# Kernel tuning notes

Measured on AMD Instinct MI355X. Metric: run time of the kernel, lower is better.

## Reference

```python
import jax, jax.numpy as jnp
import numpy as np
from jax import lax

B, T, N_INPUT = 64, 2048, 257
HIDDEN = 32
N_OUTPUT = 10


def setup_inputs() -> dict:
    key = jax.random.key(0)
    ks = jax.random.split(key, 7)
    return {
        "specs": jax.random.normal(ks[0], (B, T, N_INPUT), dtype=jnp.float32),
        "W_ih": jax.random.normal(ks[1], (4 * HIDDEN, N_INPUT), dtype=jnp.float32) * 0.05,
        "W_hh": jax.random.normal(ks[2], (4 * HIDDEN, HIDDEN), dtype=jnp.float32) * 0.05,
        "b_ih": jax.random.normal(ks[3], (4 * HIDDEN,), dtype=jnp.float32) * 0.05,
        "b_hh": jax.random.normal(ks[4], (4 * HIDDEN,), dtype=jnp.float32) * 0.05,
        "W_out": jax.random.normal(ks[5], (N_OUTPUT, HIDDEN), dtype=jnp.float32) * 0.05,
        "b_out": jax.random.normal(ks[6], (N_OUTPUT,), dtype=jnp.float32) * 0.05,
    }


def reference(specs, W_ih, W_hh, b_ih, b_hh, W_out, b_out):
    # specs: [B, T, n_input]. PyTorch LSTMCell, gate order (i, f, g, o).
    b, t, _ = specs.shape
    h0 = jnp.zeros((b, HIDDEN), dtype=specs.dtype)
    c0 = jnp.zeros((b, HIDDEN), dtype=specs.dtype)
    # Precompute input projection for all timesteps in one GEMM: [B, T, 4H]
    x_proj = jnp.einsum("bti,gi->btg", specs, W_ih) + b_ih + b_hh
    x_proj = jnp.swapaxes(x_proj, 0, 1)  # [T, B, 4H] for scan

    def step(carry, xg):
        h, c = carry
        gates = xg + h @ W_hh.T  # [B, 4H]
        i, f, g, o = jnp.split(gates, 4, axis=-1)
        i = jax.nn.sigmoid(i)
        f = jax.nn.sigmoid(f)
        g = jnp.tanh(g)
        o = jax.nn.sigmoid(o)
        c = f * c + i * g
        h = o * jnp.tanh(c)
        return (h, c), None

    (hn, _), _ = lax.scan(step, (h0, c0), x_proj)
    logits = jax.nn.relu(hn) @ W_out.T + b_out  # [B, n_output]
    return jax.nn.log_softmax(logits, axis=1)
```

## Files before the change

### kernel.cpp

```cpp
#include <hip/hip_runtime.h>

#define B_SZ 64
#define T_LEN 2048
#define NIN 257
#define HID 32
#define G4 128
#define NOUT 10

#define TBT 128
#define PAD 34
#define CH 8
#define NSCAN 64
#define NGEMMP 128
#define NTILE 1024
#define TPB 16

#define SC_SIG  -1.44269504f
#define SC_TANH -2.88539008f

typedef int v2i __attribute__((ext_vector_type(2)));
typedef unsigned long long u64;

__device__ __forceinline__ void pkfma2(float2& acc, float2 w, u64 h2) {
  asm("v_pk_fma_f32 %0, %1, %2, %0" : "+v"(acc) : "v"(w), "s"(h2));
}

__device__ __forceinline__ float2 pkadd(float2 a, float2 b) {
  float2 d;
  asm("v_pk_add_f32 %0, %1, %2" : "=v"(d) : "v"(a), "v"(b));
  return d;
}

__device__ __forceinline__ void gemm_tile(
    const float* __restrict__ A, const float* __restrict__ W,
    const float* __restrict__ b_ih, const float* __restrict__ b_hh,
    float* __restrict__ C, int bt0, float* sA, float* sB)
{
  const int tid = threadIdx.x;
  const int gt = tid & 15;
  const int btt = tid >> 4;
  float acc[8][8];
#pragma unroll
  for (int i = 0; i < 8; ++i)
#pragma unroll
    for (int j = 0; j < 8; ++j) acc[i][j] = 0.f;

  for (int kc = 0; kc < 8; ++kc) {
    const int k0 = kc * 32;
    __syncthreads();
#pragma unroll
    for (int i = 0; i < 16; ++i) {
      int s = i * 256 + tid;
      int r = s >> 5, cc = s & 31;
      sA[r * PAD + cc] = A[(size_t)(bt0 + r) * NIN + k0 + cc];
      sB[r * PAD + cc] = W[(size_t)r * NIN + k0 + cc];
    }
    __syncthreads();
#pragma unroll
    for (int k2 = 0; k2 < 16; ++k2) {
      float2 a2[8], b2[8];
#pragma unroll
      for (int i = 0; i < 8; ++i)
        a2[i] = *(const float2*)&sA[(btt + 16 * i) * PAD + 2 * k2];
#pragma unroll
      for (int j = 0; j < 8; ++j)
        b2[j] = *(const float2*)&sB[(gt + 16 * j) * PAD + 2 * k2];
#pragma unroll
      for (int i = 0; i < 8; ++i)
#pragma unroll
        for (int j = 0; j < 8; ++j) {
          acc[i][j] = fmaf(a2[i].x, b2[j].x, acc[i][j]);
          acc[i][j] = fmaf(a2[i].y, b2[j].y, acc[i][j]);
        }
    }
  }
  {
    float a[8], bb[8];
#pragma unroll
    for (int i = 0; i < 8; ++i) a[i] = A[(size_t)(bt0 + btt + 16 * i) * NIN + 256];
#pragma unroll
    for (int j = 0; j < 8; ++j) bb[j] = W[(size_t)(gt + 16 * j) * NIN + 256];
#pragma unroll
    for (int i = 0; i < 8; ++i)
#pragma unroll
      for (int j = 0; j < 8; ++j) acc[i][j] += a[i] * bb[j];
  }
  float bias[8], sc[8];
  int off[8];
#pragma unroll
  for (int j = 0; j < 8; ++j) {
    const int col = gt + 16 * j;
    bias[j] = b_ih[col] + b_hh[col];
    sc[j] = ((col >> 5) == 2) ? SC_TANH : SC_SIG;
    off[j] = ((col & 63) << 1) + (col >> 6);
  }
#pragma unroll
  for (int i = 0; i < 8; ++i) {
    size_t row = (size_t)(bt0 + btt + 16 * i) * G4;
#pragma unroll
    for (int j = 0; j < 8; ++j) C[row + off[j]] = (acc[i][j] + bias[j]) * sc[j];
  }
}

__global__ __launch_bounds__(256) void fused(
    const float* __restrict__ A,
    const float* __restrict__ W,
    const float* __restrict__ b_ih,
    const float* __restrict__ b_hh,
    const float* __restrict__ W_hh,
    const float* __restrict__ W_out,
    const float* __restrict__ b_out,
    float* __restrict__ out,
    float* __restrict__ xproj,
    int* __restrict__ flags,
    int nowait)
{
  __shared__ float sA[TBT * PAD];
  __shared__ float sB[G4 * PAD];
  const int bid = blockIdx.x;

  if (bid >= NSCAN) {
    const int p = bid - NSCAN;
    for (int idx = p; idx < NTILE; idx += NGEMMP) {
      const int ti = idx >> 6, bb = idx & 63;
      const int bt0 = bb * T_LEN + ti * TBT;
      gemm_tile(A, W, b_ih, b_hh, xproj, bt0, sA, sB);
      __threadfence();
      __syncthreads();
      if (threadIdx.x == 0)
        __hip_atomic_store(&flags[idx], 1, __ATOMIC_RELEASE, __HIP_MEMORY_SCOPE_AGENT);
    }
    return;
  }

  if (threadIdx.x >= 64) return;
  __builtin_amdgcn_s_setprio(3);
  const int b = bid;
  const int l = threadIdx.x;

  const float wsB = (l < HID) ? SC_TANH : SC_SIG;
  float2 wA[16], wB[16];
#pragma unroll
  for (int j = 0; j < 16; j += 2) {
    float4 v0 = *(const float4*)&W_hh[l * HID + 2 * j];
    wA[j]     = make_float2(v0.x * SC_SIG, v0.y * SC_SIG);
    wA[j + 1] = make_float2(v0.z * SC_SIG, v0.w * SC_SIG);
    float4 v1 = *(const float4*)&W_hh[(l + 64) * HID + 2 * j];
    wB[j]     = make_float2(v1.x * wsB, v1.y * wsB);
    wB[j + 1] = make_float2(v1.z * wsB, v1.w * wsB);
  }

  float c = 0.f, h = 0.f;
  u64 hp[16];
#pragma unroll
  for (int k = 0; k < 16; ++k) hp[k] = 0ull;

  const float2* xb2 = (const float2*)(xproj + (size_t)b * T_LEN * G4);

  auto step = [&](float xa, float xg) {
    float2 aA[4], aB[4];
    aA[0] = make_float2(xa, 0.f);
    aB[0] = make_float2(xg, 0.f);
#pragma unroll
    for (int q = 1; q < 4; ++q) {
      aA[q] = make_float2(0.f, 0.f);
      aB[q] = make_float2(0.f, 0.f);
    }
#pragma unroll
    for (int j = 0; j < 16; j += 4) {
#pragma unroll
      for (int q = 0; q < 4; ++q) {
        pkfma2(aA[q], wA[j + q], hp[j + q]);
        pkfma2(aB[q], wB[j + q], hp[j + q]);
      }
    }
    float2 tA = pkadd(pkadd(aA[0], aA[1]), pkadd(aA[2], aA[3]));
    float2 tB = pkadd(pkadd(aB[0], aB[1]), pkadd(aB[2], aB[3]));
    float accA = tA.x + tA.y;
    float accB = tB.x + tB.y;
    float actA = __builtin_amdgcn_rcpf(1.f + __builtin_amdgcn_exp2f(accA));
    float sB2  = __builtin_amdgcn_rcpf(1.f + __builtin_amdgcn_exp2f(accB));
    float actA2 = actA + actA;
    float prod  = fmaf(actA2, sB2, -actA);
    v2i sw = __builtin_amdgcn_permlane32_swap(0, __float_as_int(prod), false, false);
    float pr = __int_as_float(sw[0]);
    c = fmaf(actA, c, pr);
    float t  = __builtin_amdgcn_rcpf(1.f + __builtin_amdgcn_exp2f(SC_TANH * c));
    float s2 = sB2 + sB2;
    h = fmaf(s2, t, -sB2);
#pragma unroll
    for (int k = 0; k < 16; ++k) {
      unsigned lo = (unsigned)__builtin_amdgcn_readlane(__float_as_int(h), 32 + 2 * k);
      unsigned hi = (unsigned)__builtin_amdgcn_readlane(__float_as_int(h), 33 + 2 * k);
      hp[k] = (u64)lo | ((u64)hi << 32);
    }
  };

  float2 X0[CH], X1[CH];
#define LOADC2(X, P) do { _Pragma("unroll") \
  for (int i = 0; i < CH; ++i) X[i] = (P)[i * 64]; } while (0)
#define STEPS(X) do { _Pragma("unroll") \
  for (int i = 0; i < CH; ++i) step(X[i].x, X[i].y); } while (0)

  for (int ti = 0; ti < TPB; ++ti) {
    if (!nowait) {
      while (__hip_atomic_load(&flags[ti * 64 + b], __ATOMIC_ACQUIRE,
                               __HIP_MEMORY_SCOPE_AGENT) == 0)
        __builtin_amdgcn_s_sleep(2);
    }
    const float2* xt = xb2 + (size_t)ti * TBT * 64 + l;
    LOADC2(X0, xt);
#pragma unroll 1
    for (int ch = 0; ch < TBT / CH; ch += 2) {
      const float2* s1 = xt + (size_t)(ch + 1) * CH * 64;
      LOADC2(X1, s1);
      STEPS(X0);
      if (ch + 2 < TBT / CH) {
        const float2* s2 = xt + (size_t)(ch + 2) * CH * 64;
        LOADC2(X0, s2);
      }
      STEPS(X1);
    }
  }

  float hf[HID];
#pragma unroll
  for (int k = 0; k < HID; ++k)
    hf[k] = __int_as_float(__builtin_amdgcn_readlane(__float_as_int(h), 32 + k));
  float logit = 0.f;
  if (l < NOUT) {
    logit = b_out[l];
#pragma unroll
    for (int j = 0; j < HID; ++j) logit += fmaxf(hf[j], 0.f) * W_out[l * HID + j];
  }
  float m = -1e30f;
#pragma unroll
  for (int n = 0; n < NOUT; ++n) m = fmaxf(m, __shfl(logit, n));
  float s = 0.f;
#pragma unroll
  for (int n = 0; n < NOUT; ++n)
    s += __builtin_amdgcn_exp2f(1.44269504089f * (__shfl(logit, n) - m));
  if (l < NOUT)
    out[b * NOUT + l] = logit - m - 0.69314718056f * __builtin_amdgcn_logf(s);
}

__global__ __launch_bounds__(256) void xproj_gemm(
    const float* __restrict__ A, const float* __restrict__ W,
    const float* __restrict__ b_ih, const float* __restrict__ b_hh,
    float* __restrict__ C)
{
  __shared__ float sA[TBT * PAD];
  __shared__ float sB[G4 * PAD];
  const int idx = blockIdx.x;
  const int ti = idx >> 6, bb = idx & 63;
  gemm_tile(A, W, b_ih, b_hh, C, bb * T_LEN + ti * TBT, sA, sB);
}

extern "C" void kernel_launch(void* const* d_in, const int* in_sizes, int n_in,
                              void* d_out, int out_size, void* d_ws, size_t ws_size,
                              hipStream_t stream) {
  const float* specs = (const float*)d_in[0];
  const float* W_ih  = (const float*)d_in[1];
  const float* W_hh  = (const float*)d_in[2];
  const float* b_ih  = (const float*)d_in[3];
  const float* b_hh  = (const float*)d_in[4];
  const float* W_out = (const float*)d_in[5];
  const float* b_out = (const float*)d_in[6];
  float* outp  = (float*)d_out;
  float* xproj = (float*)d_ws;
  const size_t xbytes = (size_t)B_SZ * T_LEN * G4 * 4;

  if (ws_size >= xbytes + NTILE * sizeof(int)) {
    int* flags = (int*)((char*)d_ws + xbytes);
    (void)hipMemsetAsync(flags, 0, NTILE * sizeof(int), stream);
    fused<<<NSCAN + NGEMMP, 256, 0, stream>>>(specs, W_ih, b_ih, b_hh, W_hh,
                                              W_out, b_out, outp, xproj, flags, 0);
  } else {
    xproj_gemm<<<NTILE, 256, 0, stream>>>(specs, W_ih, b_ih, b_hh, xproj);
    fused<<<NSCAN, 256, 0, stream>>>(specs, W_ih, b_ih, b_hh, W_hh,
                                     W_out, b_out, outp, xproj, (int*)xproj , 1);
  }
}
```

Baseline: 565.9 us.

## Use fp16 dot2 for recurrent matvec and halve h broadcast readlanes

Converts the pre-scaled recurrent weights and the broadcast hidden state to packed fp16 and replaces the packed fp32 FMAs with v_dot2_f32_f16, so each instruction handles two products with fp32 accumulation. A DPP move pairs neighbouring h values before packing, which cuts the per-step readlane count from 32 to 16. The cell state is kept pre-scaled so the tanh argument needs no multiply. This shortens the serial per-timestep chain but lowers the precision of h and W_hh to fp16, which may cause accuracy drift over 2048 steps.

```diff
diff --git a/kernel.cpp b/kernel.cpp
--- a/kernel.cpp
+++ b/kernel.cpp
@@ -21,15 +21,11 @@
 typedef int v2i __attribute__((ext_vector_type(2)));
 typedef unsigned long long u64;
 
-__device__ __forceinline__ void pkfma2(float2& acc, float2 w, u64 h2) {
-  asm("v_pk_fma_f32 %0, %1, %2, %0" : "+v"(acc) : "v"(w), "s"(h2));
-}
-
-__device__ __forceinline__ float2 pkadd(float2 a, float2 b) {
-  float2 d;
-  asm("v_pk_add_f32 %0, %1, %2" : "=v"(d) : "v"(a), "v"(b));
-  return d;
-}
+#define DOT2(acc, w, hpk) \
+  asm("v_dot2_f32_f16 %0, %1, %2, %0" : "+v"(acc) : "v"(w), "s"(hpk))
+
+#define PKF16(dst, a, b) \
+  asm("v_cvt_pkrtz_f16_f32 %0, %1, %2" : "=v"(dst) : "v"(a), "v"(b))
 
 __device__ __forceinline__ void gemm_tile(
     const float* __restrict__ A, const float* __restrict__ W,
@@ -139,61 +135,57 @@
   const int l = threadIdx.x;
 
   const float wsB = (l < HID) ? SC_TANH : SC_SIG;
-  float2 wA[16], wB[16];
+  unsigned wA[16], wB[16];
 #pragma unroll
   for (int j = 0; j < 16; j += 2) {
     float4 v0 = *(const float4*)&W_hh[l * HID + 2 * j];
-    wA[j]     = make_float2(v0.x * SC_SIG, v0.y * SC_SIG);
-    wA[j + 1] = make_float2(v0.z * SC_SIG, v0.w * SC_SIG);
+    PKF16(wA[j],     v0.x * SC_SIG, v0.y * SC_SIG);
+    PKF16(wA[j + 1], v0.z * SC_SIG, v0.w * SC_SIG);
     float4 v1 = *(const float4*)&W_hh[(l + 64) * HID + 2 * j];
-    wB[j]     = make_float2(v1.x * wsB, v1.y * wsB);
-    wB[j + 1] = make_float2(v1.z * wsB, v1.w * wsB);
+    PKF16(wB[j],     v1.x * wsB, v1.y * wsB);
+    PKF16(wB[j + 1], v1.z * wsB, v1.w * wsB);
   }
 
   float c = 0.f, h = 0.f;
-  u64 hp[16];
-#pragma unroll
-  for (int k = 0; k < 16; ++k) hp[k] = 0ull;
+  unsigned hp[16];
+#pragma unroll
+  for (int k = 0; k < 16; ++k) hp[k] = 0u;
 
   const float2* xb2 = (const float2*)(xproj + (size_t)b * T_LEN * G4);
 
   auto step = [&](float xa, float xg) {
-    float2 aA[4], aB[4];
-    aA[0] = make_float2(xa, 0.f);
-    aB[0] = make_float2(xg, 0.f);
-#pragma unroll
-    for (int q = 1; q < 4; ++q) {
-      aA[q] = make_float2(0.f, 0.f);
-      aB[q] = make_float2(0.f, 0.f);
-    }
-#pragma unroll
-    for (int j = 0; j < 16; j += 4) {
-#pragma unroll
-      for (int q = 0; q < 4; ++q) {
-        pkfma2(aA[q], wA[j + q], hp[j + q]);
-        pkfma2(aB[q], wB[j + q], hp[j + q]);
-      }
-    }
-    float2 tA = pkadd(pkadd(aA[0], aA[1]), pkadd(aA[2], aA[3]));
-    float2 tB = pkadd(pkadd(aB[0], aB[1]), pkadd(aB[2], aB[3]));
-    float accA = tA.x + tA.y;
-    float accB = tB.x + tB.y;
+    float aA0 = xa,  aA1 = 0.f, aA2 = 0.f, aA3 = 0.f;
+    float aB0 = xg,  aB1 = 0.f, aB2 = 0.f, aB3 = 0.f;
+#pragma unroll
+    for (int j = 0; j < 4; ++j) {
+      DOT2(aA0, wA[j],      hp[j]);
+      DOT2(aA1, wA[4 + j],  hp[4 + j]);
+      DOT2(aA2, wA[8 + j],  hp[8 + j]);
+      DOT2(aA3, wA[12 + j], hp[12 + j]);
+      DOT2(aB0, wB[j],      hp[j]);
+      DOT2(aB1, wB[4 + j],  hp[4 + j]);
+      DOT2(aB2, wB[8 + j],  hp[8 + j]);
+      DOT2(aB3, wB[12 + j], hp[12 + j]);
+    }
+    float accA = (aA0 + aA1) + (aA2 + aA3);
+    float accB = (aB0 + aB1) + (aB2 + aB3);
     float actA = __builtin_amdgcn_rcpf(1.f + __builtin_amdgcn_exp2f(accA));
     float sB2  = __builtin_amdgcn_rcpf(1.f + __builtin_amdgcn_exp2f(accB));
-    float actA2 = actA + actA;
-    float prod  = fmaf(actA2, sB2, -actA);
+    float m1 = actA * (2.f * SC_TANH);
+    float sh = sB2 - 0.5f;
+    float prod = m1 * sh;
     v2i sw = __builtin_amdgcn_permlane32_swap(0, __float_as_int(prod), false, false);
     float pr = __int_as_float(sw[0]);
     c = fmaf(actA, c, pr);
-    float t  = __builtin_amdgcn_rcpf(1.f + __builtin_amdgcn_exp2f(SC_TANH * c));
+    float t  = __builtin_amdgcn_rcpf(1.f + __builtin_amdgcn_exp2f(c));
     float s2 = sB2 + sB2;
     h = fmaf(s2, t, -sB2);
-#pragma unroll
-    for (int k = 0; k < 16; ++k) {
-      unsigned lo = (unsigned)__builtin_amdgcn_readlane(__float_as_int(h), 32 + 2 * k);
-      unsigned hi = (unsigned)__builtin_amdgcn_readlane(__float_as_int(h), 33 + 2 * k);
-      hp[k] = (u64)lo | ((u64)hi << 32);
-    }
+    int hn = __builtin_amdgcn_mov_dpp(__float_as_int(h), 0xF5, 0xF, 0xF, false);
+    int pk;
+    PKF16(pk, h, __int_as_float(hn));
+#pragma unroll
+    for (int k = 0; k < 16; ++k)
+      hp[k] = (unsigned)__builtin_amdgcn_readlane(pk, 32 + 2 * k);
   };
 
   float2 X0[CH], X1[CH];
```

After: 568.2 us. About the same (+0.4%).
